# Kernel tuning notes

Hardware: AMD Instinct MI355X
Metric: run time of the kernel (lower is better)

The kernel has to match this reference:

```python
import jax, jax.numpy as jnp
import numpy as np

D = 4       # number of TT dimensions
N = 128     # mode size per dimension (Ns)
R = 16      # TT rank (RMAX)
B = 262144  # batch of query points


def setup_inputs() -> dict:
    key = jax.random.key(0)
    ks = jax.random.split(key, 5)
    # points in [-1, 1] (remap_needed=True assumes this domain)
    x = jax.random.uniform(ks[0], (B, D), dtype=jnp.float32) * 2.0 - 1.0
    core0 = jax.random.normal(ks[1], (1, N, R), dtype=jnp.float32)
    core1 = jax.random.normal(ks[2], (R, N, R), dtype=jnp.float32)
    core2 = jax.random.normal(ks[3], (R, N, R), dtype=jnp.float32)
    core3 = jax.random.normal(ks[4], (R, N, 1), dtype=jnp.float32)
    return {"x": x, "core0": core0, "core1": core1, "core2": core2, "core3": core3}


def _forward(x, cores):
    # remap: (x + 1) / 2 * (Ns[0] - 1)  (module uses Ns[0] for all dims)
    n0 = cores[0].shape[1]
    xr = (x + 1.0) * 0.5 * (n0 - 1)
    # per-dim clamp to [0, Ns[i]-1]
    ns = jnp.array([c.shape[1] for c in cores], dtype=x.dtype)  # [D]
    xc = jnp.clip(xr, 0.0, ns - 1.0)  # broadcast over D
    idx_low = jnp.floor(xc).astype(jnp.int32)   # [B, D]
    idx_high = jnp.ceil(xc).astype(jnp.int32)   # [B, D]
    wh = xc - idx_low.astype(x.dtype)           # [B, D] interpolation weights
    # gather + linear interpolation per core -> list of [r_prev, B, r_next]
    newcores = []
    for i, c in enumerate(cores):
        lo = jnp.take(c, idx_low[:, i], axis=1)   # [r_prev, B, r_next]
        hi = jnp.take(c, idx_high[:, i], axis=1)  # [r_prev, B, r_next]
        w = wh[:, i][None, :, None]               # [1, B, 1]
        newcores.append((1.0 - w) * lo + w * hi)
    # chained batched contraction, right to left (matches ttcontract)
    res = newcores[-1]
    for i in range(len(newcores) - 2, 0, -1):
        res = jnp.einsum('abc,cbk->abk', newcores[i], res)
    return jnp.einsum('abc,cbk->b', newcores[0], res)  # [B]


def reference(x, core0, core1, core2, core3):
    return _forward(x, [core0, core1, core2, core3])
```

## Files before the change

kernel.cpp:

```cpp
#include <hip/hip_runtime.h>
#include <hip/hip_bf16.h>

typedef unsigned int uint32;
typedef unsigned short u16;

#define NPT 128
#define RNK 16
#define MIDROW 264
#define MIDROW_U32 132
#define EDGEROW 20
#define SMEM_BYTES (2*NPT*MIDROW*2 + 2*NPT*EDGEROW*4)

#if defined(__has_builtin)
#if __has_builtin(__builtin_amdgcn_fdot2_f32_bf16)
#define HAVE_BFDOT2 1
#endif
#endif

__device__ __forceinline__ float bl(uint32 u){ return __uint_as_float(u << 16); }
__device__ __forceinline__ float bh(uint32 u){ return __uint_as_float(u & 0xffff0000u); }

#ifdef HAVE_BFDOT2
typedef __bf16 v2bf __attribute__((ext_vector_type(2)));
__device__ __forceinline__ v2bf bc(uint32 u){ return __builtin_bit_cast(v2bf, u); }

__device__ __forceinline__ float dot16b(const uint32* vp, uint4 U0, uint4 U1) {
  float s0 = 0.f, s1 = 0.f;
  s0 = __builtin_amdgcn_fdot2_f32_bf16(bc(vp[0]), bc(U0.x), s0, false);
  s0 = __builtin_amdgcn_fdot2_f32_bf16(bc(vp[1]), bc(U0.y), s0, false);
  s0 = __builtin_amdgcn_fdot2_f32_bf16(bc(vp[2]), bc(U0.z), s0, false);
  s0 = __builtin_amdgcn_fdot2_f32_bf16(bc(vp[3]), bc(U0.w), s0, false);
  s1 = __builtin_amdgcn_fdot2_f32_bf16(bc(vp[4]), bc(U1.x), s1, false);
  s1 = __builtin_amdgcn_fdot2_f32_bf16(bc(vp[5]), bc(U1.y), s1, false);
  s1 = __builtin_amdgcn_fdot2_f32_bf16(bc(vp[6]), bc(U1.z), s1, false);
  s1 = __builtin_amdgcn_fdot2_f32_bf16(bc(vp[7]), bc(U1.w), s1, false);
  return s0 + s1;
}
#else
__device__ __forceinline__ float dot16(const float* v, uint4 U0, uint4 U1) {
  float s0 = fmaf(v[1],  bh(U0.x), v[0]*bl(U0.x));
  s0 = fmaf(v[2],  bl(U0.y), s0); s0 = fmaf(v[3],  bh(U0.y), s0);
  float s1 = fmaf(v[5],  bh(U0.z), v[4]*bl(U0.z));
  s1 = fmaf(v[6],  bl(U0.w), s1); s1 = fmaf(v[7],  bh(U0.w), s1);
  float s2 = fmaf(v[9],  bh(U1.x), v[8]*bl(U1.x));
  s2 = fmaf(v[10], bl(U1.y), s2); s2 = fmaf(v[11], bh(U1.y), s2);
  float s3 = fmaf(v[13], bh(U1.z), v[12]*bl(U1.z));
  s3 = fmaf(v[14], bl(U1.w), s3); s3 = fmaf(v[15], bh(U1.w), s3);
  return (s0 + s1) + (s2 + s3);
}
#endif

__device__ __forceinline__ void tt_mid(const uint32* __restrict__ base, float xc, float v[16]) {
  int n0 = (int)xc;
  float w = xc - (float)n0;
  int n1 = min(n0 + 1, NPT - 1);
  const uint32* r0 = base + n0 * MIDROW_U32;
  const uint32* r1 = base + n1 * MIDROW_U32;

#ifdef HAVE_BFDOT2
  uint32 vp[8];
#pragma unroll
  for (int k = 0; k < 8; ++k) {
    __hip_bfloat16 l = __float2bfloat16(v[2*k]);
    __hip_bfloat16 h = __float2bfloat16(v[2*k+1]);
    vp[k] = (uint32)(*(u16*)&l) | ((uint32)(*(u16*)&h) << 16);
  }
#endif

  float nv[16];
#pragma unroll
  for (int j = 0; j < 16; ++j) {
    const uint4* p0 = (const uint4*)(r0 + j * 8);
    const uint4* p1 = (const uint4*)(r1 + j * 8);
    uint4 A0 = p0[0], A1 = p0[1];
    uint4 B0 = p1[0], B1 = p1[1];
#ifdef HAVE_BFDOT2
    float a = dot16b(vp, A0, A1);
    float b = dot16b(vp, B0, B1);
#else
    float a = dot16(v, A0, A1);
    float b = dot16(v, B0, B1);
#endif
    nv[j] = fmaf(w, b - a, a);
  }
#pragma unroll
  for (int j = 0; j < 16; ++j) v[j] = nv[j];
}

__device__ __forceinline__ float remap_clamp(float x) {
  float xr = (x + 1.0f) * 0.5f * (float)(NPT - 1);
  return fminf(fmaxf(xr, 0.0f), (float)(NPT - 1));
}

__global__ __launch_bounds__(1024, 4) void tt_kernel(
    const float* __restrict__ x,  const float* __restrict__ g0,
    const float* __restrict__ g1, const float* __restrict__ g2,
    const float* __restrict__ g3, float* __restrict__ out, int npts)
{
  extern __shared__ char smem[];
  unsigned short* c1 = (unsigned short*)smem;
  unsigned short* c2 = c1 + NPT * MIDROW;
  float* c0 = (float*)(c2 + NPT * MIDROW);
  float* c3 = c0 + NPT * EDGEROW;

  for (int t = threadIdx.x; t < RNK * NPT * RNK; t += blockDim.x) {
    int i = t >> 11;
    int n = (t >> 4) & (NPT - 1);
    int j = t & (RNK - 1);
    __hip_bfloat16 h1 = __float2bfloat16(g1[t]);
    __hip_bfloat16 h2 = __float2bfloat16(g2[t]);
    c1[n * MIDROW + j * 16 + i] = *(u16*)&h1;
    c2[n * MIDROW + j * 16 + i] = *(u16*)&h2;
  }
  for (int t = threadIdx.x; t < NPT * RNK; t += blockDim.x) {
    int n = t >> 4;
    int i = t & (RNK - 1);
    c0[n * EDGEROW + i] = g0[t];
    c3[n * EDGEROW + i] = g3[i * NPT + n];
  }
  __syncthreads();

  int p = blockIdx.x * blockDim.x + threadIdx.x;
  if (p >= npts) return;
  float4 xv = reinterpret_cast<const float4*>(x)[p];

  float v[16];
  {
    float xc = remap_clamp(xv.x);
    int n0 = (int)xc; float w = xc - (float)n0; int n1 = min(n0 + 1, NPT - 1);
    const float4* L = (const float4*)(c0 + n0 * EDGEROW);
    const float4* H = (const float4*)(c0 + n1 * EDGEROW);
#pragma unroll
    for (int k = 0; k < 4; ++k) {
      float4 l = L[k], h = H[k];
      v[4*k+0] = fmaf(w, h.x - l.x, l.x);
      v[4*k+1] = fmaf(w, h.y - l.y, l.y);
      v[4*k+2] = fmaf(w, h.z - l.z, l.z);
      v[4*k+3] = fmaf(w, h.w - l.w, l.w);
    }
  }
  tt_mid((const uint32*)c1, remap_clamp(xv.y), v);
  tt_mid((const uint32*)c2, remap_clamp(xv.z), v);
  float acc;
  {
    float xc = remap_clamp(xv.w);
    int n0 = (int)xc; float w = xc - (float)n0; int n1 = min(n0 + 1, NPT - 1);
    const float4* L = (const float4*)(c3 + n0 * EDGEROW);
    const float4* H = (const float4*)(c3 + n1 * EDGEROW);
    float a0 = 0.f, a1 = 0.f, a2 = 0.f, a3 = 0.f;
#pragma unroll
    for (int k = 0; k < 4; ++k) {
      float4 l = L[k], h = H[k];
      a0 = fmaf(v[4*k+0], fmaf(w, h.x - l.x, l.x), a0);
      a1 = fmaf(v[4*k+1], fmaf(w, h.y - l.y, l.y), a1);
      a2 = fmaf(v[4*k+2], fmaf(w, h.z - l.z, l.z), a2);
      a3 = fmaf(v[4*k+3], fmaf(w, h.w - l.w, l.w), a3);
    }
    acc = (a0 + a1) + (a2 + a3);
  }
  out[p] = acc;
}

extern "C" void kernel_launch(void* const* d_in, const int* in_sizes, int n_in,
                              void* d_out, int out_size, void* d_ws, size_t ws_size,
                              hipStream_t stream) {
  const float* x  = (const float*)d_in[0];
  const float* g0 = (const float*)d_in[1];
  const float* g1 = (const float*)d_in[2];
  const float* g2 = (const float*)d_in[3];
  const float* g3 = (const float*)d_in[4];
  float* out = (float*)d_out;

  int B = in_sizes[0] / 4;
  hipFuncSetAttribute(reinterpret_cast<const void*>(tt_kernel),
                      hipFuncAttributeMaxDynamicSharedMemorySize, SMEM_BYTES);
  int block = 1024;
  int grid = (B + block - 1) / block;
  tt_kernel<<<grid, block, SMEM_BYTES, stream>>>(x, g0, g1, g2, g3, out, B);
}
```

Before: 83.48 us.

## Overlap core2 staging with core1 contraction and vectorize swizzled LDS staging

Each thread now loads core data with vectorized float2 global reads, packs 8 bf16 values into uint4 stores, and writes them into LDS rows with an XOR swizzle on the j-slot. Core2 is loaded into registers before the first contraction and written to LDS after it, with a second barrier, so its load latency overlaps the core1 compute. Core0 is read straight from global memory instead of LDS, which shrinks the shared memory footprint. The cost is extra live registers for the staged data, an added barrier, and swizzle index math inside the hot loop.

```diff
diff --git a/kernel.cpp b/kernel.cpp
--- a/kernel.cpp
+++ b/kernel.cpp
@@ -8,8 +8,8 @@
 #define RNK 16
 #define MIDROW 264
 #define MIDROW_U32 132
-#define EDGEROW 20
-#define SMEM_BYTES (2*NPT*MIDROW*2 + 2*NPT*EDGEROW*4)
+#define EROW 20
+#define SMEM_BYTES (2*NPT*MIDROW*2 + NPT*EROW*4)
 
 #if defined(__has_builtin)
 #if __has_builtin(__builtin_amdgcn_fdot2_f32_bf16)
@@ -19,6 +19,12 @@
 
 __device__ __forceinline__ float bl(uint32 u){ return __uint_as_float(u << 16); }
 __device__ __forceinline__ float bh(uint32 u){ return __uint_as_float(u & 0xffff0000u); }
+
+__device__ __forceinline__ uint32 pk2(float a, float b){
+  __hip_bfloat16 l = __float2bfloat16(a);
+  __hip_bfloat16 h = __float2bfloat16(b);
+  return (uint32)(*(u16*)&l) | ((uint32)(*(u16*)&h) << 16);
+}
 
 #ifdef HAVE_BFDOT2
 typedef __bf16 v2bf __attribute__((ext_vector_type(2)));
@@ -50,28 +56,49 @@
 }
 #endif
 
+__device__ __forceinline__ float remap_clamp(float x) {
+  float xr = (x + 1.0f) * 0.5f * (float)(NPT - 1);
+  return fminf(fmaxf(xr, 0.0f), (float)(NPT - 1));
+}
+
+__device__ __forceinline__ void stage_loads(const float* __restrict__ g, int t, float2* f) {
+  int n = t >> 4, q = (t >> 1) & 7, h = t & 1;
+  const float* s = g + (h * 8) * 2048 + n * 16 + q * 2;
+#pragma unroll
+  for (int k = 0; k < 8; ++k) f[k] = *(const float2*)(s + k * 2048);
+}
+__device__ __forceinline__ void stage_write(u16* __restrict__ dst, int t, const float2* f) {
+  int n = t >> 4, q = (t >> 1) & 7, h = t & 1;
+  int sw = (n >> 3) & 3;
+  int j0 = 2 * q, j1 = 2 * q + 1;
+  uint4 w0, w1;
+  w0.x = pk2(f[0].x, f[1].x); w0.y = pk2(f[2].x, f[3].x);
+  w0.z = pk2(f[4].x, f[5].x); w0.w = pk2(f[6].x, f[7].x);
+  w1.x = pk2(f[0].y, f[1].y); w1.y = pk2(f[2].y, f[3].y);
+  w1.z = pk2(f[4].y, f[5].y); w1.w = pk2(f[6].y, f[7].y);
+  *(uint4*)(dst + n * MIDROW + ((j0 ^ sw) << 4) + h * 8) = w0;
+  *(uint4*)(dst + n * MIDROW + ((j1 ^ sw) << 4) + h * 8) = w1;
+}
+
 __device__ __forceinline__ void tt_mid(const uint32* __restrict__ base, float xc, float v[16]) {
   int n0 = (int)xc;
   float w = xc - (float)n0;
   int n1 = min(n0 + 1, NPT - 1);
   const uint32* r0 = base + n0 * MIDROW_U32;
   const uint32* r1 = base + n1 * MIDROW_U32;
+  int s0w = (n0 >> 3) & 3, s1w = (n1 >> 3) & 3;
 
 #ifdef HAVE_BFDOT2
   uint32 vp[8];
 #pragma unroll
-  for (int k = 0; k < 8; ++k) {
-    __hip_bfloat16 l = __float2bfloat16(v[2*k]);
-    __hip_bfloat16 h = __float2bfloat16(v[2*k+1]);
-    vp[k] = (uint32)(*(u16*)&l) | ((uint32)(*(u16*)&h) << 16);
-  }
+  for (int k = 0; k < 8; ++k) vp[k] = pk2(v[2*k], v[2*k+1]);
 #endif
 
   float nv[16];
 #pragma unroll
   for (int j = 0; j < 16; ++j) {
-    const uint4* p0 = (const uint4*)(r0 + j * 8);
-    const uint4* p1 = (const uint4*)(r1 + j * 8);
+    const uint4* p0 = (const uint4*)(r0 + ((j ^ s0w) << 3));
+    const uint4* p1 = (const uint4*)(r1 + ((j ^ s1w) << 3));
     uint4 A0 = p0[0], A1 = p0[1];
     uint4 B0 = p1[0], B1 = p1[1];
 #ifdef HAVE_BFDOT2
@@ -87,49 +114,42 @@
   for (int j = 0; j < 16; ++j) v[j] = nv[j];
 }
 
-__device__ __forceinline__ float remap_clamp(float x) {
-  float xr = (x + 1.0f) * 0.5f * (float)(NPT - 1);
-  return fminf(fmaxf(xr, 0.0f), (float)(NPT - 1));
-}
-
 __global__ __launch_bounds__(1024, 4) void tt_kernel(
     const float* __restrict__ x,  const float* __restrict__ g0,
     const float* __restrict__ g1, const float* __restrict__ g2,
     const float* __restrict__ g3, float* __restrict__ out, int npts)
 {
   extern __shared__ char smem[];
-  unsigned short* c1 = (unsigned short*)smem;
-  unsigned short* c2 = c1 + NPT * MIDROW;
-  float* c0 = (float*)(c2 + NPT * MIDROW);
-  float* c3 = c0 + NPT * EDGEROW;
-
-  for (int t = threadIdx.x; t < RNK * NPT * RNK; t += blockDim.x) {
-    int i = t >> 11;
-    int n = (t >> 4) & (NPT - 1);
-    int j = t & (RNK - 1);
-    __hip_bfloat16 h1 = __float2bfloat16(g1[t]);
-    __hip_bfloat16 h2 = __float2bfloat16(g2[t]);
-    c1[n * MIDROW + j * 16 + i] = *(u16*)&h1;
-    c2[n * MIDROW + j * 16 + i] = *(u16*)&h2;
-  }
-  for (int t = threadIdx.x; t < NPT * RNK; t += blockDim.x) {
-    int n = t >> 4;
-    int i = t & (RNK - 1);
-    c0[n * EDGEROW + i] = g0[t];
-    c3[n * EDGEROW + i] = g3[i * NPT + n];
-  }
-  __syncthreads();
-
-  int p = blockIdx.x * blockDim.x + threadIdx.x;
-  if (p >= npts) return;
+  u16* c1   = (u16*)smem;
+  u16* c2   = c1 + NPT * MIDROW;
+  float* e3 = (float*)(c2 + NPT * MIDROW);
+
+  const int tid = (int)threadIdx.x;
+  const int p0i = (int)blockIdx.x * 1024 + tid;
+  const int p   = min(p0i, npts - 1);
+
   float4 xv = reinterpret_cast<const float4*>(x)[p];
+
+  float2 f1a[8], f1b[8];
+  stage_loads(g1, tid, f1a);
+  stage_loads(g1, tid + 1024, f1b);
+
+  int en0 = tid >> 4,          ei0 = tid & 15;
+  int en1 = (tid + 1024) >> 4, ei1 = (tid + 1024) & 15;
+  float ev0 = g3[ei0 * NPT + en0];
+  float ev1 = g3[ei1 * NPT + en1];
+
+  stage_write(c1, tid, f1a);
+  stage_write(c1, tid + 1024, f1b);
+  e3[en0 * EROW + ei0] = ev0;
+  e3[en1 * EROW + ei1] = ev1;
 
   float v[16];
   {
     float xc = remap_clamp(xv.x);
     int n0 = (int)xc; float w = xc - (float)n0; int n1 = min(n0 + 1, NPT - 1);
-    const float4* L = (const float4*)(c0 + n0 * EDGEROW);
-    const float4* H = (const float4*)(c0 + n1 * EDGEROW);
+    const float4* L = (const float4*)(g0 + n0 * 16);
+    const float4* H = (const float4*)(g0 + n1 * 16);
 #pragma unroll
     for (int k = 0; k < 4; ++k) {
       float4 l = L[k], h = H[k];
@@ -139,14 +159,28 @@
       v[4*k+3] = fmaf(w, h.w - l.w, l.w);
     }
   }
+
+  float2 f2a[8], f2b[8];
+  stage_loads(g2, tid, f2a);
+  stage_loads(g2, tid + 1024, f2b);
+
+  __syncthreads();
+
   tt_mid((const uint32*)c1, remap_clamp(xv.y), v);
+
+  stage_write(c2, tid, f2a);
+  stage_write(c2, tid + 1024, f2b);
+
+  __syncthreads();
+
   tt_mid((const uint32*)c2, remap_clamp(xv.z), v);
+
   float acc;
   {
     float xc = remap_clamp(xv.w);
     int n0 = (int)xc; float w = xc - (float)n0; int n1 = min(n0 + 1, NPT - 1);
-    const float4* L = (const float4*)(c3 + n0 * EDGEROW);
-    const float4* H = (const float4*)(c3 + n1 * EDGEROW);
+    const float4* L = (const float4*)(e3 + n0 * EROW);
+    const float4* H = (const float4*)(e3 + n1 * EROW);
     float a0 = 0.f, a1 = 0.f, a2 = 0.f, a3 = 0.f;
 #pragma unroll
     for (int k = 0; k < 4; ++k) {
@@ -158,7 +192,7 @@
     }
     acc = (a0 + a1) + (a2 + a3);
   }
-  out[p] = acc;
+  if (p0i < npts) out[p0i] = acc;
 }
 
 extern "C" void kernel_launch(void* const* d_in, const int* in_sizes, int n_in,
```

Result: slower. 130.7 us (+56.6%).
